# Optimization experiments

Measured on AMD Instinct MI355X. Metric: run time of the kernel, lower is better.

## Reference

```python
import jax, jax.numpy as jnp
import numpy as np

EVENTLEN = 8  # config.event_length
NEG = -10000.0


def setup_inputs() -> dict:
    key = jax.random.key(0)
    k1, k2 = jax.random.split(key)
    T, B, E = 128, 512, 128  # decodelen, batch_size, entity_size
    feats = jax.random.normal(k1, (T, B, E), dtype=jnp.float32)
    transitions = jax.random.normal(k2, (E, E), dtype=jnp.float32)
    # Same masking the torch module applies to transitions.data at init
    transitions = transitions.at[0, :].set(NEG).at[:, -1].set(NEG)
    return {"feats": feats, "transitions": transitions}


def reference(feats, transitions):
    """Segmented CRF forward algorithm (OneCrfCCKSDecoder._forward_alg).

    feats:       [T, B, E] per-step emission scores (entity tag logits)
    transitions: [E, E]    transitions[j, k] = score of k -> j
    Returns scalar alpha / (T // EVENTLEN).
    """
    T, B, E = feats.shape
    n_events = T // EVENTLEN

    # Faithful to torch: init_alphas[:][0] = 0.0 zeroes the batch-0 ROW.
    init_fv = jnp.full((B, E), NEG, dtype=feats.dtype).at[0].set(0.0)

    t_idx = jnp.arange(T)
    is_boundary = (t_idx % EVENTLEN == 0) & (t_idx != 0)  # accumulate alpha
    is_update = (t_idx % EVENTLEN != 0)                   # DP update step

    def step(carry, inp):
        fv, alpha = carry              # fv: [B, E], alpha: scalar
        feat, bnd, upd = inp           # feat: [B, E]
        # Event-boundary accumulation (uses fv BEFORE any update; note the
        # original never resets fv inside _forward_alg).
        alpha_inc = jnp.mean(jax.nn.logsumexp(fv + transitions[-1], axis=1))
        alpha = alpha + jnp.where(bnd, alpha_inc, jnp.zeros_like(alpha_inc))
        # fv_new[b, j] = logsumexp_k( fv[b,k] + feat[b,k] + transitions[j,k] )
        x = fv + feat                                        # [B, E]
        fv_new = jax.nn.logsumexp(x[:, None, :] + transitions[None, :, :], axis=-1)
        fv = jnp.where(upd, fv_new, fv)
        return (fv, alpha), None

    (fv, alpha), _ = jax.lax.scan(
        step, (init_fv, jnp.zeros((), feats.dtype)), (feats, is_boundary, is_update)
    )
    # Terminal accumulation after the loop.
    alpha = alpha + jnp.mean(jax.nn.logsumexp(fv + transitions[-1], axis=1))
    return alpha / n_events
```

## Files before the change

kernel.cpp:

```cpp
#include <hip/hip_runtime.h>


typedef _Float16 f16x4 __attribute__((ext_vector_type(4)));
typedef _Float16 f16x8 __attribute__((ext_vector_type(8)));
typedef float    f32x4 __attribute__((ext_vector_type(4)));

#define NEG_VAL   (-10000.0f)
#define C_SCALE   0.0024787521766663585f
#define LOG_C     6.0f

#define LDS_BARRIER() asm volatile("s_waitcnt lgkmcnt(0)\n\ts_barrier" ::: "memory")

__device__ __align__(16) _Float16 g_ef[128 * 512 * 128];

__global__ __launch_bounds__(256)
void prep_exp(const float* __restrict__ feats)
{
    int id = blockIdx.x * 256 + threadIdx.x;
    #pragma unroll
    for (int it = 0; it < 4; ++it, id += 524288) {
        const int jj = id & 31;
        const int tb = id >> 5;
        const int b  = tb & 511;
        const int t  = tb >> 9;
        f32x4 x = *(const f32x4*)(feats + (size_t)tb * 128 + 4 * jj);
        auto lo = __builtin_amdgcn_cvt_pkrtz(__expf(x[0]) * C_SCALE,
                                             __expf(x[1]) * C_SCALE);
        auto hi = __builtin_amdgcn_cvt_pkrtz(__expf(x[2]) * C_SCALE,
                                             __expf(x[3]) * C_SCALE);
        f16x4 o;
        o[0] = (_Float16)lo[0]; o[1] = (_Float16)lo[1];
        o[2] = (_Float16)hi[0]; o[3] = (_Float16)hi[1];
        const int off = t * 65536 + (b >> 4) * 2048 + (jj >> 2) * 256
                      + (b & 15) * 16 + (jj & 3) * 4;
        *(f16x4*)(g_ef + off) = o;
    }
}

__device__ inline f16x4 cvt4(f32x4 a) {
    auto lo = __builtin_amdgcn_cvt_pkrtz(a[0], a[1]);
    auto hi = __builtin_amdgcn_cvt_pkrtz(a[2], a[3]);
    f16x4 o;
    o[0] = (_Float16)lo[0]; o[1] = (_Float16)lo[1];
    o[2] = (_Float16)hi[0]; o[3] = (_Float16)hi[1];
    return o;
}

__global__ __launch_bounds__(512)
void crf_fwd(const float* __restrict__ trans,
             float* __restrict__ out)
{
    const int tid  = threadIdx.x;
    const int w    = tid >> 6;
    const int lane = tid & 63;
    const int bloc = lane & 15;
    const int q    = lane >> 4;
    const int b    = blockIdx.x * 16 + bloc;

    f16x8 Afrag[4];
    {
        const float* rowp = trans + (size_t)(16 * w + bloc) * 128;
        #pragma unroll
        for (int kap = 0; kap < 4; ++kap) {
            const f32x4* p = (const f32x4*)(rowp + 32 * kap + 8 * q);
            f32x4 x = p[0], y = p[1];
            f16x8 f;
            f[0] = (_Float16)__expf(x[0]); f[1] = (_Float16)__expf(x[1]);
            f[2] = (_Float16)__expf(x[2]); f[3] = (_Float16)__expf(x[3]);
            f[4] = (_Float16)__expf(y[0]); f[5] = (_Float16)__expf(y[1]);
            f[6] = (_Float16)__expf(y[2]); f[7] = (_Float16)__expf(y[3]);
            Afrag[kap] = f;
        }
    }
    f32x4 te;
    {
        f32x4 x = *(const f32x4*)(trans + 127 * 128 + 16 * w + 4 * q);
        te[0] = __expf(x[0]); te[1] = __expf(x[1]);
        te[2] = __expf(x[2]); te[3] = __expf(x[3]);
    }

    __shared__ __align__(16) char  Hbuf[8192];
    __shared__ float Spart[16 * 8];
    __shared__ float Mpart[16 * 8];

    const int waddr = bloc * 256 + (((2 * w + (q >> 1)) ^ bloc) * 16) + 8 * (q & 1);
    int raddr[4];
    #pragma unroll
    for (int kap = 0; kap < 4; ++kap)
        raddr[kap] = bloc * 256 + (((4 * kap + q) ^ bloc) * 16);

    const _Float16* efb = g_ef + blockIdx.x * 2048 + w * 256 + bloc * 16 + q * 4;
    f16x4 cur, nx1, nx2;
    cur = *(const f16x4*)(efb + 1 * 65536);
    nx1 = *(const f16x4*)(efb + 2 * 65536);
    nx2 = *(const f16x4*)(efb + 3 * 65536);

    f32x4 acc = {1.f, 1.f, 1.f, 1.f};
    float M     = (b == 0) ? 0.0f : NEG_VAL;
    float alpha = 0.0f;
    int hb = 0;

    #pragma unroll 8
    for (int t = 1; t < 128; ++t) {
        const bool upd = (t & 7) != 0;

        if (upd) {
            M += LOG_C;
            f16x4 hh = cvt4(acc) * cur;
            *(f16x4*)(Hbuf + hb + waddr) = hh;
            LDS_BARRIER();

            f16x8 B0 = *(const f16x8*)(Hbuf + hb + raddr[0]);
            f16x8 B1 = *(const f16x8*)(Hbuf + hb + raddr[1]);
            f16x8 B2 = *(const f16x8*)(Hbuf + hb + raddr[2]);
            f16x8 B3 = *(const f16x8*)(Hbuf + hb + raddr[3]);

            f32x4 z = {0.f, 0.f, 0.f, 0.f};
            f32x4 da = __builtin_amdgcn_mfma_f32_16x16x32_f16(Afrag[0], B0, z, 0, 0, 0);
            f32x4 db = __builtin_amdgcn_mfma_f32_16x16x32_f16(Afrag[1], B1, z, 0, 0, 0);
            da = __builtin_amdgcn_mfma_f32_16x16x32_f16(Afrag[2], B2, da, 0, 0, 0);
            db = __builtin_amdgcn_mfma_f32_16x16x32_f16(Afrag[3], B3, db, 0, 0, 0);
            acc = da + db;
            hb ^= 4096;
        } else {
            float s = acc[0] * te[0] + acc[1] * te[1]
                    + acc[2] * te[2] + acc[3] * te[3];
            float m = fmaxf(fmaxf(acc[0], acc[1]), fmaxf(acc[2], acc[3]));
            s += __shfl_xor(s, 16, 64);
            s += __shfl_xor(s, 32, 64);
            m = fmaxf(m, __shfl_xor(m, 16, 64));
            m = fmaxf(m, __shfl_xor(m, 32, 64));
            if (q == 0) {
                Spart[bloc * 8 + w] = s;
                Mpart[bloc * 8 + w] = m;
            }
            LDS_BARRIER();

            f32x4 sa = *(const f32x4*)&Spart[bloc * 8];
            f32x4 sb = *(const f32x4*)&Spart[bloc * 8 + 4];
            f32x4 ma = *(const f32x4*)&Mpart[bloc * 8];
            f32x4 mb = *(const f32x4*)&Mpart[bloc * 8 + 4];
            float r = ((sa[0] + sa[1]) + (sa[2] + sa[3]))
                    + ((sb[0] + sb[1]) + (sb[2] + sb[3]));
            float cmax = fmaxf(fmaxf(fmaxf(ma[0], ma[1]), fmaxf(ma[2], ma[3])),
                               fmaxf(fmaxf(mb[0], mb[1]), fmaxf(mb[2], mb[3])));

            alpha += M + __logf(r);
            const float inv = __builtin_amdgcn_rcpf(cmax);
            acc[0] *= inv; acc[1] *= inv; acc[2] *= inv; acc[3] *= inv;
            M += __logf(cmax);
        }

        if (t + 1 < 128) {
            cur = nx1;
            nx1 = nx2;
            if (t + 3 < 128) nx2 = *(const f16x4*)(efb + (size_t)(t + 3) * 65536);
        }
    }

    {
        float s = acc[0] * te[0] + acc[1] * te[1]
                + acc[2] * te[2] + acc[3] * te[3];
        s += __shfl_xor(s, 16, 64);
        s += __shfl_xor(s, 32, 64);
        if (q == 0) Spart[bloc * 8 + w] = s;
        LDS_BARRIER();
        f32x4 sa = *(const f32x4*)&Spart[bloc * 8];
        f32x4 sb = *(const f32x4*)&Spart[bloc * 8 + 4];
        float r = ((sa[0] + sa[1]) + (sa[2] + sa[3]))
                + ((sb[0] + sb[1]) + (sb[2] + sb[3]));
        alpha += M + __logf(r);
    }

    if (w == 0) {
        float v = alpha;
        #pragma unroll
        for (int off = 1; off < 64; off <<= 1)
            v += __shfl_xor(v, off, 64);
        if (lane == 0)
            atomicAdd(out, v * (1.0f / (4.0f * 512.0f * 16.0f)));
    }
}

extern "C" void kernel_launch(void* const* d_in, const int* in_sizes, int n_in,
                              void* d_out, int out_size, void* d_ws, size_t ws_size,
                              hipStream_t stream) {
    const float* feats = (const float*)d_in[0];
    const float* trans = (const float*)d_in[1];
    float* out = (float*)d_out;

    (void)hipMemsetAsync(out, 0, sizeof(float), stream);
    prep_exp<<<2048, 256, 0, stream>>>(feats);
    crf_fwd<<<32, 512, 0, stream>>>(trans, out);
}
```

Measured before the change: 107.5 us.

## Halve waves per CRF block, each wave computing two output tiles

The CRF recurrence kernel now runs 4 waves per block instead of 8. Each wave owns two 16-row tiles of the transition matrix and issues 8 MFMAs per step while reusing the same B fragments from LDS. This cuts the number of waves taking part in each per-step barrier and halves the cross-wave partial-sum reduction. In exchange, each wave does twice the serial MFMA and conversion work per step, which lengthens the per-step critical path.

Measured after the change: 115.7 us. 7.6% more time.

```diff
diff --git a/kernel.cpp b/kernel.cpp
--- a/kernel.cpp
+++ b/kernel.cpp
@@ -46,7 +46,7 @@
     return o;
 }
 
-__global__ __launch_bounds__(512)
+__global__ __launch_bounds__(256, 1)
 void crf_fwd(const float* __restrict__ trans,
              float* __restrict__ out)
 {
@@ -57,9 +57,12 @@
     const int q    = lane >> 4;
     const int b    = blockIdx.x * 16 + bloc;
 
-    f16x8 Afrag[4];
-    {
-        const float* rowp = trans + (size_t)(16 * w + bloc) * 128;
+    f16x8 Afrag[2][4];
+    f32x4 te[2];
+    #pragma unroll
+    for (int jj = 0; jj < 2; ++jj) {
+        const int jt = 2 * w + jj;
+        const float* rowp = trans + (size_t)(16 * jt + bloc) * 128;
         #pragma unroll
         for (int kap = 0; kap < 4; ++kap) {
             const f32x4* p = (const f32x4*)(rowp + 32 * kap + 8 * q);
@@ -69,33 +72,40 @@
             f[2] = (_Float16)__expf(x[2]); f[3] = (_Float16)__expf(x[3]);
             f[4] = (_Float16)__expf(y[0]); f[5] = (_Float16)__expf(y[1]);
             f[6] = (_Float16)__expf(y[2]); f[7] = (_Float16)__expf(y[3]);
-            Afrag[kap] = f;
+            Afrag[jj][kap] = f;
         }
-    }
-    f32x4 te;
-    {
-        f32x4 x = *(const f32x4*)(trans + 127 * 128 + 16 * w + 4 * q);
-        te[0] = __expf(x[0]); te[1] = __expf(x[1]);
-        te[2] = __expf(x[2]); te[3] = __expf(x[3]);
+        f32x4 x = *(const f32x4*)(trans + 127 * 128 + 16 * jt + 4 * q);
+        te[jj][0] = __expf(x[0]); te[jj][1] = __expf(x[1]);
+        te[jj][2] = __expf(x[2]); te[jj][3] = __expf(x[3]);
     }
 
     __shared__ __align__(16) char  Hbuf[8192];
-    __shared__ float Spart[16 * 8];
-    __shared__ float Mpart[16 * 8];
-
-    const int waddr = bloc * 256 + (((2 * w + (q >> 1)) ^ bloc) * 16) + 8 * (q & 1);
-    int raddr[4];
+    __shared__ float Spart[16 * 4];
+    __shared__ float Mpart[16 * 4];
+
+    int waddr[2], raddr[4];
+    #pragma unroll
+    for (int jj = 0; jj < 2; ++jj) {
+        const int jt = 2 * w + jj;
+        waddr[jj] = bloc * 256 + (((2 * jt + (q >> 1)) ^ bloc) * 16) + 8 * (q & 1);
+    }
     #pragma unroll
     for (int kap = 0; kap < 4; ++kap)
         raddr[kap] = bloc * 256 + (((4 * kap + q) ^ bloc) * 16);
 
-    const _Float16* efb = g_ef + blockIdx.x * 2048 + w * 256 + bloc * 16 + q * 4;
-    f16x4 cur, nx1, nx2;
-    cur = *(const f16x4*)(efb + 1 * 65536);
-    nx1 = *(const f16x4*)(efb + 2 * 65536);
-    nx2 = *(const f16x4*)(efb + 3 * 65536);
-
-    f32x4 acc = {1.f, 1.f, 1.f, 1.f};
+    const _Float16* efb0 = g_ef + blockIdx.x * 2048 + (2 * w)     * 256 + bloc * 16 + q * 4;
+    const _Float16* efb1 = g_ef + blockIdx.x * 2048 + (2 * w + 1) * 256 + bloc * 16 + q * 4;
+    f16x4 cur[2], nx1[2], nx2[2];
+    cur[0] = *(const f16x4*)(efb0 + 1 * 65536);
+    cur[1] = *(const f16x4*)(efb1 + 1 * 65536);
+    nx1[0] = *(const f16x4*)(efb0 + 2 * 65536);
+    nx1[1] = *(const f16x4*)(efb1 + 2 * 65536);
+    nx2[0] = *(const f16x4*)(efb0 + 3 * 65536);
+    nx2[1] = *(const f16x4*)(efb1 + 3 * 65536);
+
+    f32x4 acc[2];
+    acc[0] = (f32x4){1.f, 1.f, 1.f, 1.f};
+    acc[1] = (f32x4){1.f, 1.f, 1.f, 1.f};
     float M     = (b == 0) ? 0.0f : NEG_VAL;
     float alpha = 0.0f;
     int hb = 0;
@@ -106,8 +116,10 @@
 
         if (upd) {
             M += LOG_C;
-            f16x4 hh = cvt4(acc) * cur;
-            *(f16x4*)(Hbuf + hb + waddr) = hh;
+            f16x4 hh0 = cvt4(acc[0]) * cur[0];
+            f16x4 hh1 = cvt4(acc[1]) * cur[1];
+            *(f16x4*)(Hbuf + hb + waddr[0]) = hh0;
+            *(f16x4*)(Hbuf + hb + waddr[1]) = hh1;
             LDS_BARRIER();
 
             f16x8 B0 = *(const f16x8*)(Hbuf + hb + raddr[0]);
@@ -116,59 +128,69 @@
             f16x8 B3 = *(const f16x8*)(Hbuf + hb + raddr[3]);
 
             f32x4 z = {0.f, 0.f, 0.f, 0.f};
-            f32x4 da = __builtin_amdgcn_mfma_f32_16x16x32_f16(Afrag[0], B0, z, 0, 0, 0);
-            f32x4 db = __builtin_amdgcn_mfma_f32_16x16x32_f16(Afrag[1], B1, z, 0, 0, 0);
-            da = __builtin_amdgcn_mfma_f32_16x16x32_f16(Afrag[2], B2, da, 0, 0, 0);
-            db = __builtin_amdgcn_mfma_f32_16x16x32_f16(Afrag[3], B3, db, 0, 0, 0);
-            acc = da + db;
+            f32x4 da0 = __builtin_amdgcn_mfma_f32_16x16x32_f16(Afrag[0][0], B0, z, 0, 0, 0);
+            f32x4 db0 = __builtin_amdgcn_mfma_f32_16x16x32_f16(Afrag[0][1], B1, z, 0, 0, 0);
+            f32x4 da1 = __builtin_amdgcn_mfma_f32_16x16x32_f16(Afrag[1][0], B0, z, 0, 0, 0);
+            f32x4 db1 = __builtin_amdgcn_mfma_f32_16x16x32_f16(Afrag[1][1], B1, z, 0, 0, 0);
+            da0 = __builtin_amdgcn_mfma_f32_16x16x32_f16(Afrag[0][2], B2, da0, 0, 0, 0);
+            db0 = __builtin_amdgcn_mfma_f32_16x16x32_f16(Afrag[0][3], B3, db0, 0, 0, 0);
+            da1 = __builtin_amdgcn_mfma_f32_16x16x32_f16(Afrag[1][2], B2, da1, 0, 0, 0);
+            db1 = __builtin_amdgcn_mfma_f32_16x16x32_f16(Afrag[1][3], B3, db1, 0, 0, 0);
+            acc[0] = da0 + db0;
+            acc[1] = da1 + db1;
             hb ^= 4096;
         } else {
-            float s = acc[0] * te[0] + acc[1] * te[1]
-                    + acc[2] * te[2] + acc[3] * te[3];
-            float m = fmaxf(fmaxf(acc[0], acc[1]), fmaxf(acc[2], acc[3]));
+            float s = acc[0][0] * te[0][0] + acc[0][1] * te[0][1]
+                    + acc[0][2] * te[0][2] + acc[0][3] * te[0][3]
+                    + acc[1][0] * te[1][0] + acc[1][1] * te[1][1]
+                    + acc[1][2] * te[1][2] + acc[1][3] * te[1][3];
+            float m = fmaxf(fmaxf(fmaxf(acc[0][0], acc[0][1]),
+                                  fmaxf(acc[0][2], acc[0][3])),
+                            fmaxf(fmaxf(acc[1][0], acc[1][1]),
+                                  fmaxf(acc[1][2], acc[1][3])));
             s += __shfl_xor(s, 16, 64);
             s += __shfl_xor(s, 32, 64);
             m = fmaxf(m, __shfl_xor(m, 16, 64));
             m = fmaxf(m, __shfl_xor(m, 32, 64));
             if (q == 0) {
-                Spart[bloc * 8 + w] = s;
-                Mpart[bloc * 8 + w] = m;
+                Spart[bloc * 4 + w] = s;
+                Mpart[bloc * 4 + w] = m;
             }
             LDS_BARRIER();
 
-            f32x4 sa = *(const f32x4*)&Spart[bloc * 8];
-            f32x4 sb = *(const f32x4*)&Spart[bloc * 8 + 4];
-            f32x4 ma = *(const f32x4*)&Mpart[bloc * 8];
-            f32x4 mb = *(const f32x4*)&Mpart[bloc * 8 + 4];
-            float r = ((sa[0] + sa[1]) + (sa[2] + sa[3]))
-                    + ((sb[0] + sb[1]) + (sb[2] + sb[3]));
-            float cmax = fmaxf(fmaxf(fmaxf(ma[0], ma[1]), fmaxf(ma[2], ma[3])),
-                               fmaxf(fmaxf(mb[0], mb[1]), fmaxf(mb[2], mb[3])));
+            f32x4 sa = *(const f32x4*)&Spart[bloc * 4];
+            f32x4 ma = *(const f32x4*)&Mpart[bloc * 4];
+            float r    = (sa[0] + sa[1]) + (sa[2] + sa[3]);
+            float cmax = fmaxf(fmaxf(ma[0], ma[1]), fmaxf(ma[2], ma[3]));
 
             alpha += M + __logf(r);
             const float inv = __builtin_amdgcn_rcpf(cmax);
-            acc[0] *= inv; acc[1] *= inv; acc[2] *= inv; acc[3] *= inv;
+            acc[0][0] *= inv; acc[0][1] *= inv; acc[0][2] *= inv; acc[0][3] *= inv;
+            acc[1][0] *= inv; acc[1][1] *= inv; acc[1][2] *= inv; acc[1][3] *= inv;
             M += __logf(cmax);
         }
 
         if (t + 1 < 128) {
-            cur = nx1;
-            nx1 = nx2;
-            if (t + 3 < 128) nx2 = *(const f16x4*)(efb + (size_t)(t + 3) * 65536);
+            cur[0] = nx1[0]; cur[1] = nx1[1];
+            nx1[0] = nx2[0]; nx1[1] = nx2[1];
+            if (t + 3 < 128) {
+                nx2[0] = *(const f16x4*)(efb0 + (size_t)(t + 3) * 65536);
+                nx2[1] = *(const f16x4*)(efb1 + (size_t)(t + 3) * 65536);
+            }
         }
     }
 
     {
-        float s = acc[0] * te[0] + acc[1] * te[1]
-                + acc[2] * te[2] + acc[3] * te[3];
+        float s = acc[0][0] * te[0][0] + acc[0][1] * te[0][1]
+                + acc[0][2] * te[0][2] + acc[0][3] * te[0][3]
+                + acc[1][0] * te[1][0] + acc[1][1] * te[1][1]
+                + acc[1][2] * te[1][2] + acc[1][3] * te[1][3];
         s += __shfl_xor(s, 16, 64);
         s += __shfl_xor(s, 32, 64);
-        if (q == 0) Spart[bloc * 8 + w] = s;
+        if (q == 0) Spart[bloc * 4 + w] = s;
         LDS_BARRIER();
-        f32x4 sa = *(const f32x4*)&Spart[bloc * 8];
-        f32x4 sb = *(const f32x4*)&Spart[bloc * 8 + 4];
-        float r = ((sa[0] + sa[1]) + (sa[2] + sa[3]))
-                + ((sb[0] + sb[1]) + (sb[2] + sb[3]));
+        f32x4 sa = *(const f32x4*)&Spart[bloc * 4];
+        float r = (sa[0] + sa[1]) + (sa[2] + sa[3]);
         alpha += M + __logf(r);
     }
 
@@ -191,5 +213,5 @@
 
     (void)hipMemsetAsync(out, 0, sizeof(float), stream);
     prep_exp<<<2048, 256, 0, stream>>>(feats);
-    crf_fwd<<<32, 512, 0, stream>>>(trans, out);
-}
+    crf_fwd<<<32, 256, 0, stream>>>(trans, out);
+}
```

## Fuse exp prep into CRF kernel with producer blocks overlapping the recurrence

Applied to the files above, without the earlier changes.

Merges the separate exp/fp16 conversion kernel and the CRF scan into one launch. 32 engine blocks run the recurrence and compute exp for the first time slices inline from fp32 feats. 1024 producer blocks convert the later slices into the fp16 buffer and signal completion through a global atomic counter. Engines poll the counter once at step 40 and fall back to inline conversion if the producers have not finished. This hides the prep kernel's runtime and launch gap behind the serial recurrence, at the cost of spin-wait logic, counter-reset handshaking, and possible contention for CUs between producers and engines.

New measurement: 204.2 us. 89.9% more time.

```diff
diff --git a/kernel.cpp b/kernel.cpp
--- a/kernel.cpp
+++ b/kernel.cpp
@@ -8,34 +8,16 @@
 #define NEG_VAL   (-10000.0f)
 #define C_SCALE   0.0024787521766663585f
 #define LOG_C     6.0f
+#define NENG      32
+#define NPROD     1024
+#define SLICE0    44
+#define WAIT_T    40
+#define SPIN_MAX  16384
 
 #define LDS_BARRIER() asm volatile("s_waitcnt lgkmcnt(0)\n\ts_barrier" ::: "memory")
 
 __device__ __align__(16) _Float16 g_ef[128 * 512 * 128];
-
-__global__ __launch_bounds__(256)
-void prep_exp(const float* __restrict__ feats)
-{
-    int id = blockIdx.x * 256 + threadIdx.x;
-    #pragma unroll
-    for (int it = 0; it < 4; ++it, id += 524288) {
-        const int jj = id & 31;
-        const int tb = id >> 5;
-        const int b  = tb & 511;
-        const int t  = tb >> 9;
-        f32x4 x = *(const f32x4*)(feats + (size_t)tb * 128 + 4 * jj);
-        auto lo = __builtin_amdgcn_cvt_pkrtz(__expf(x[0]) * C_SCALE,
-                                             __expf(x[1]) * C_SCALE);
-        auto hi = __builtin_amdgcn_cvt_pkrtz(__expf(x[2]) * C_SCALE,
-                                             __expf(x[3]) * C_SCALE);
-        f16x4 o;
-        o[0] = (_Float16)lo[0]; o[1] = (_Float16)lo[1];
-        o[2] = (_Float16)hi[0]; o[3] = (_Float16)hi[1];
-        const int off = t * 65536 + (b >> 4) * 2048 + (jj >> 2) * 256
-                      + (b & 15) * 16 + (jj & 3) * 4;
-        *(f16x4*)(g_ef + off) = o;
-    }
-}
+__device__ int g_done = 0;
 
 __device__ inline f16x4 cvt4(f32x4 a) {
     auto lo = __builtin_amdgcn_cvt_pkrtz(a[0], a[1]);
@@ -46,11 +28,48 @@
     return o;
 }
 
-__global__ __launch_bounds__(512)
-void crf_fwd(const float* __restrict__ trans,
-             float* __restrict__ out)
+__device__ inline f16x4 expC4(f32x4 x) {
+    f32x4 e;
+    e[0] = __expf(x[0]) * C_SCALE; e[1] = __expf(x[1]) * C_SCALE;
+    e[2] = __expf(x[2]) * C_SCALE; e[3] = __expf(x[3]) * C_SCALE;
+    return cvt4(e);
+}
+
+__global__ __launch_bounds__(512, 1)
+void crf_fused(const float* __restrict__ feats,
+               const float* __restrict__ trans,
+               float* __restrict__ out)
 {
-    const int tid  = threadIdx.x;
+    const int tid = threadIdx.x;
+
+    if (blockIdx.x >= NENG) {
+        const int pid = (blockIdx.x - NENG) * 512 + tid;
+        #pragma unroll
+        for (int it = 0; it < 3; ++it) {
+            const int c = it * (NPROD * 512) + pid;
+            if (c < (128 - SLICE0) * 16384) {
+                const int s  = SLICE0 + (c >> 14);
+                const int u  = c & 16383;
+                const int jj = u & 31;
+                const int b  = u >> 5;
+                f32x4 x = *(const f32x4*)(feats + ((size_t)s * 512 + b) * 128 + 4 * jj);
+                f16x4 o = expC4(x);
+                const int off = s * 65536 + (b >> 4) * 2048 + (jj >> 2) * 256
+                              + (b & 15) * 16 + (jj & 3) * 4;
+                *(f16x4*)(g_ef + off) = o;
+            }
+        }
+        asm volatile("s_waitcnt vmcnt(0)" ::: "memory");
+        __syncthreads();
+        if (tid == 0) {
+            __threadfence();
+            __hip_atomic_fetch_add(&g_done, 1, __ATOMIC_RELEASE,
+                                   __HIP_MEMORY_SCOPE_AGENT);
+        }
+        return;
+    }
+
+    __builtin_amdgcn_s_setprio(1);
     const int w    = tid >> 6;
     const int lane = tid & 63;
     const int bloc = lane & 15;
@@ -82,6 +101,7 @@
     __shared__ __align__(16) char  Hbuf[8192];
     __shared__ float Spart[16 * 8];
     __shared__ float Mpart[16 * 8];
+    __shared__ int   sh_efok;
 
     const int waddr = bloc * 256 + (((2 * w + (q >> 1)) ^ bloc) * 16) + 8 * (q & 1);
     int raddr[4];
@@ -89,11 +109,13 @@
     for (int kap = 0; kap < 4; ++kap)
         raddr[kap] = bloc * 256 + (((4 * kap + q) ^ bloc) * 16);
 
+    const float*    fb  = feats + (size_t)b * 128 + 16 * w + 4 * q;
     const _Float16* efb = g_ef + blockIdx.x * 2048 + w * 256 + bloc * 16 + q * 4;
     f16x4 cur, nx1, nx2;
-    cur = *(const f16x4*)(efb + 1 * 65536);
-    nx1 = *(const f16x4*)(efb + 2 * 65536);
-    nx2 = *(const f16x4*)(efb + 3 * 65536);
+    cur = expC4(*(const f32x4*)(fb + 1 * 65536));
+    nx1 = expC4(*(const f32x4*)(fb + 2 * 65536));
+    nx2 = expC4(*(const f32x4*)(fb + 3 * 65536));
+    int efok = 1;
 
     f32x4 acc = {1.f, 1.f, 1.f, 1.f};
     float M     = (b == 0) ? 0.0f : NEG_VAL;
@@ -134,6 +156,19 @@
                 Spart[bloc * 8 + w] = s;
                 Mpart[bloc * 8 + w] = m;
             }
+            if (t == WAIT_T && tid == 0) {
+                int ok = 0;
+                for (int spin = 0; spin < SPIN_MAX; ++spin) {
+                    if (__hip_atomic_load(&g_done, __ATOMIC_ACQUIRE,
+                                          __HIP_MEMORY_SCOPE_AGENT) >= NPROD) {
+                        ok = 1;
+                        break;
+                    }
+                    __builtin_amdgcn_s_sleep(8);
+                }
+                sh_efok = ok;
+                __threadfence();
+            }
             LDS_BARRIER();
 
             f32x4 sa = *(const f32x4*)&Spart[bloc * 8];
@@ -149,12 +184,24 @@
             const float inv = __builtin_amdgcn_rcpf(cmax);
             acc[0] *= inv; acc[1] *= inv; acc[2] *= inv; acc[3] *= inv;
             M += __logf(cmax);
+
+            if (t == WAIT_T) {
+                efok = sh_efok;
+                if (tid == 0)
+                    __hip_atomic_fetch_add(&g_done, 1, __ATOMIC_RELAXED,
+                                           __HIP_MEMORY_SCOPE_AGENT);
+            }
         }
 
         if (t + 1 < 128) {
             cur = nx1;
             nx1 = nx2;
-            if (t + 3 < 128) nx2 = *(const f16x4*)(efb + (size_t)(t + 3) * 65536);
+            if (t + 3 < 128) {
+                if (t + 3 < SLICE0 || !efok)
+                    nx2 = expC4(*(const f32x4*)(fb + (size_t)(t + 3) * 65536));
+                else
+                    nx2 = *(const f16x4*)(efb + (size_t)(t + 3) * 65536);
+            }
         }
     }
 
@@ -180,6 +227,17 @@
         if (lane == 0)
             atomicAdd(out, v * (1.0f / (4.0f * 512.0f * 16.0f)));
     }
+
+    if (blockIdx.x == 0 && tid == 0) {
+        for (int spin = 0; spin < SPIN_MAX; ++spin) {
+            if (__hip_atomic_load(&g_done, __ATOMIC_RELAXED,
+                                  __HIP_MEMORY_SCOPE_AGENT) >= NPROD + NENG)
+                break;
+            __builtin_amdgcn_s_sleep(8);
+        }
+        __hip_atomic_store(&g_done, 0, __ATOMIC_RELAXED,
+                           __HIP_MEMORY_SCOPE_AGENT);
+    }
 }
 
 extern "C" void kernel_launch(void* const* d_in, const int* in_sizes, int n_in,
@@ -190,6 +248,5 @@
     float* out = (float*)d_out;
 
     (void)hipMemsetAsync(out, 0, sizeof(float), stream);
-    prep_exp<<<2048, 256, 0, stream>>>(feats);
-    crf_fwd<<<32, 512, 0, stream>>>(trans, out);
-}
+    crf_fused<<<NENG + NPROD, 512, 0, stream>>>(feats, trans, out);
+}
```
